# Kernel optimization log

Hardware: AMD Instinct MI355X
Metric: run time of the kernel (lower is better)

The kernel has to match this reference:

```python
import jax, jax.numpy as jnp
import numpy as np

V, T, E, H, B, S = 50000, 45, 256, 512, 32, 256


def setup_inputs() -> dict:
    key = jax.random.key(0)
    ks = jax.random.split(key, 14)
    s = 0.05
    return dict(
        x=jax.random.randint(ks[0], (B, S), 0, V),
        tags=jax.random.randint(ks[1], (B, S), 0, T),
        mask=jnp.ones((B, S), dtype=bool),
        emb=jax.random.normal(ks[2], (V, E), jnp.float32),
        Wih_f=jax.random.normal(ks[3], (4 * H, E), jnp.float32) * s,
        Whh_f=jax.random.normal(ks[4], (4 * H, H), jnp.float32) * s,
        bih_f=jnp.zeros((4 * H,), jnp.float32),
        bhh_f=jnp.zeros((4 * H,), jnp.float32),
        Wih_b=jax.random.normal(ks[5], (4 * H, E), jnp.float32) * s,
        Whh_b=jax.random.normal(ks[6], (4 * H, H), jnp.float32) * s,
        bih_b=jnp.zeros((4 * H,), jnp.float32),
        bhh_b=jnp.zeros((4 * H,), jnp.float32),
        Wout=jax.random.normal(ks[7], (T, 2 * H), jnp.float32) * s,
        bout=jnp.zeros((T,), jnp.float32),
        start=jax.random.normal(ks[8], (T,), jnp.float32) * 0.1,
        end=jax.random.normal(ks[9], (T,), jnp.float32) * 0.1,
        trans=jax.random.normal(ks[10], (T, T), jnp.float32) * 0.1,
    )


def _lstm_dir(xp, Whh, reverse):
    # xp: [S, B, 4H] precomputed input projection + biases; gate order i,f,g,o (torch)
    Bn = xp.shape[1]
    Hn = Whh.shape[1]
    def step(carry, g_in):
        h, c = carry
        g = g_in + h @ Whh.T
        i, f, gg, o = jnp.split(g, 4, axis=-1)
        c = jax.nn.sigmoid(f) * c + jax.nn.sigmoid(i) * jnp.tanh(gg)
        h = jax.nn.sigmoid(o) * jnp.tanh(c)
        return (h, c), h
    init = (jnp.zeros((Bn, Hn), xp.dtype), jnp.zeros((Bn, Hn), xp.dtype))
    _, hs = jax.lax.scan(step, init, xp, reverse=reverse)
    return hs  # [S, B, H]


def _crf_nll(emissions, tags, mask, start, end, trans):
    # emissions: [B, S, T]; neg mean log-likelihood (torchcrf, reduction='mean')
    mf = mask.astype(emissions.dtype)
    em_tag = jnp.take_along_axis(emissions, tags[:, :, None], axis=2)[:, :, 0]  # [B,S]
    num = start[tags[:, 0]] + em_tag[:, 0]
    num = num + ((trans[tags[:, :-1], tags[:, 1:]] + em_tag[:, 1:]) * mf[:, 1:]).sum(1)
    seq_ends = mf.sum(1).astype(tags.dtype) - 1
    last_tags = jnp.take_along_axis(tags, seq_ends[:, None], axis=1)[:, 0]
    num = num + end[last_tags]
    def denom_step(alpha, inp):
        em_t, m_t = inp  # [B,T], [B]
        nxt = jax.nn.logsumexp(alpha[:, :, None] + trans[None, :, :] + em_t[:, None, :], axis=1)
        return jnp.where(m_t[:, None] > 0, nxt, alpha), None
    alpha0 = start[None, :] + emissions[:, 0]
    em_rest = emissions.transpose(1, 0, 2)[1:]  # [S-1, B, T]
    alpha, _ = jax.lax.scan(denom_step, alpha0, (em_rest, mf.T[1:]))
    logZ = jax.nn.logsumexp(alpha + end[None, :], axis=1)
    return -(num - logZ).mean()


def reference(x, tags, mask, emb, Wih_f, Whh_f, bih_f, bhh_f,
              Wih_b, Whh_b, bih_b, bhh_b, Wout, bout, start, end, trans):
    embeds = emb[x]                      # [B, S, E]
    xs = embeds.transpose(1, 0, 2)       # [S, B, E]
    xp_f = jnp.einsum('sbe,ge->sbg', xs, Wih_f) + bih_f + bhh_f
    hs_f = _lstm_dir(xp_f, Whh_f, False)
    xp_b = jnp.einsum('sbe,ge->sbg', xs, Wih_b) + bih_b + bhh_b
    hs_b = _lstm_dir(xp_b, Whh_b, True)
    hcat = jnp.concatenate([hs_f, hs_b], axis=-1)          # [S, B, 2H]
    emissions = jnp.einsum('sbh,th->sbt', hcat, Wout) + bout
    emissions = emissions.transpose(1, 0, 2)                # [B, S, T]
    return _crf_nll(emissions, tags, mask, start, end, trans)
```

## Files before the change

### kernel.cpp

```cpp
#include <hip/hip_runtime.h>
#include <stdint.h>

#define S_LEN 256
#define B_N 32
#define H_N 512
#define E_N 256
#define T_N 45
#define G4H 2048

typedef unsigned short u16;
typedef unsigned int u32;
typedef u16 u16x8 __attribute__((ext_vector_type(8)));
typedef u16 u16x4 __attribute__((ext_vector_type(4)));
typedef u32 u32x4 __attribute__((ext_vector_type(4)));
typedef u32 u32x2 __attribute__((ext_vector_type(2)));
typedef __bf16 bf16x8 __attribute__((ext_vector_type(8)));
typedef float f32x4 __attribute__((ext_vector_type(4)));
typedef unsigned long long u64;

#define OFF_ATOK  256ull
#define OFF_WIHF  (OFF_ATOK + 4194304ull)
#define OFF_WIHB  (OFF_WIHF + 1048576ull)
#define OFF_WHHF  (OFF_WIHB + 1048576ull)
#define OFF_WHHB  (OFF_WHHF + 2097152ull)
#define OFF_WOUT  (OFF_WHHB + 2097152ull)
#define OFF_BSF   (OFF_WOUT + 98304ull)
#define OFF_BSB   (OFF_BSF + 8192ull)
#define OFF_XPF   (OFF_BSB + 8192ull)
#define OFF_XPB   (OFF_XPF + 33554432ull)
#define OFF_HSF   (OFF_XPB + 33554432ull)
#define OFF_HSB   (OFF_HSF + 8421376ull)
#define OFF_EM    (OFF_HSB + 8421376ull)

__device__ __forceinline__ u16 f2bf(float f) {
  union { float f; unsigned u; } v; v.f = f;
  unsigned r = v.u + 0x7FFFu + ((v.u >> 16) & 1u);
  return (u16)(r >> 16);
}
__device__ __forceinline__ float bf2f(u16 b) {
  union { unsigned u; float f; } v; v.u = ((unsigned)b) << 16;
  return v.f;
}
__device__ __forceinline__ bf16x8 ld8(const u16* p) {
  u16x8 v = *reinterpret_cast<const u16x8*>(p);
  return __builtin_bit_cast(bf16x8, v);
}
__device__ __forceinline__ void st_h8cc(u16* p, u16x4 v) {
  __hip_atomic_store(reinterpret_cast<u64*>(p), __builtin_bit_cast(u64, v),
                     __ATOMIC_RELAXED, __HIP_MEMORY_SCOPE_AGENT);
}
__device__ __forceinline__ u32x4 ld16cc(const u16* p) {
  u32x4 r;
  asm volatile("global_load_dwordx4 %0, %1, off sc1"
               : "=v"(r) : "v"(p) : "memory");
  return r;
}
__device__ __forceinline__ u32x2 ld8cc(const u16* p) {
  u32x2 r;
  asm volatile("global_load_dwordx2 %0, %1, off sc1"
               : "=v"(r) : "v"(p) : "memory");
  return r;
}
__device__ __forceinline__ u32 ld4cc(const float* p) {
  u32 r;
  asm volatile("global_load_dword %0, %1, off sc1"
               : "=v"(r) : "v"(p) : "memory");
  return r;
}
__device__ __forceinline__ void st2cc(u16* p, u32 v) {
  asm volatile("global_store_short %0, %1, off sc1"
               :: "v"(p), "v"(v) : "memory");
}
__device__ __forceinline__ void st4cc(float* p, float v) {
  asm volatile("global_store_dword %0, %1, off sc1"
               :: "v"(p), "v"(__builtin_bit_cast(u32, v)) : "memory");
}
__device__ __forceinline__ f32x4 mfma16(bf16x8 a, bf16x8 b, f32x4 c) {
  return __builtin_amdgcn_mfma_f32_16x16x32_bf16(a, b, c, 0, 0, 0);
}
__device__ __forceinline__ float sigm(float x) { return 1.f / (1.f + __expf(-x)); }
__device__ __forceinline__ float tanhf_(float x) {
  float ax = fabsf(x);
  float e = __expf(-2.f * ax);
  float t = 1.f - 2.f * e / (1.f + e);
  return (x < 0.f) ? -t : t;
}
__device__ __forceinline__ float wredmax(float v) {
  #pragma unroll
  for (int m = 1; m < 64; m <<= 1) v = fmaxf(v, __shfl_xor(v, m));
  return v;
}
__device__ __forceinline__ float wredsum(float v) {
  #pragma unroll
  for (int m = 1; m < 64; m <<= 1) v += __shfl_xor(v, m);
  return v;
}

__global__ void k_castAW(const int* __restrict__ x, const float* __restrict__ emb,
                         u16* __restrict__ atok,
                         const float* __restrict__ WihF, const float* __restrict__ WihB,
                         const float* __restrict__ WhhF, const float* __restrict__ WhhB,
                         const float* __restrict__ Wout,
                         const float* __restrict__ bihF, const float* __restrict__ bhhF,
                         const float* __restrict__ bihB, const float* __restrict__ bhhB,
                         u16* wihf, u16* wihb, u16* whhf, u16* whhb, u16* woutp,
                         float* bsf, float* bsb, u16* hsf, u16* hsb,
                         u16* hsfill, u16* xpfill, float* emfill, float* outp) {
  int bid = blockIdx.x;
  if (bid >= 34512) { if (threadIdx.x == 0) *outp = 0.f; return; }
  u32x4 sent = {0xFFFFFFFFu, 0xFFFFFFFFu, 0xFFFFFFFFu, 0xFFFFFFFFu};
  if (bid >= 34128) {
    reinterpret_cast<u32x4*>(emfill)[(size_t)(bid - 34128) * 256 + threadIdx.x] = sent;
    return;
  }
  if (bid >= 17744) {
    reinterpret_cast<u32x4*>(xpfill)[(size_t)(bid - 17744) * 256 + threadIdx.x] = sent;
    return;
  }
  if (bid >= 13648) {
    reinterpret_cast<u32x4*>(hsfill)[(size_t)(bid - 13648) * 256 + threadIdx.x] = sent;
    return;
  }
  if (bid < 1024) {
    int idx = bid * 256 + threadIdx.x;
    int t = idx >> 5;
    int e0 = (idx & 31) << 3;
    int s = t >> 5, b = t & 31;
    int xid = x[b * S_LEN + s];
    const float4* p = reinterpret_cast<const float4*>(emb + (size_t)xid * E_N + e0);
    float4 lo = p[0], hi = p[1];
    u16x8 o;
    o[0] = f2bf(lo.x); o[1] = f2bf(lo.y); o[2] = f2bf(lo.z); o[3] = f2bf(lo.w);
    o[4] = f2bf(hi.x); o[5] = f2bf(hi.y); o[6] = f2bf(hi.z); o[7] = f2bf(hi.w);
    *reinterpret_cast<u16x8*>(atok + (size_t)t * E_N + e0) = o;
    return;
  }
  int i = (bid - 1024) * 256 + threadIdx.x;
  if (i < 524288) { wihf[i] = f2bf(WihF[i]); return; }
  i -= 524288;
  if (i < 524288) { wihb[i] = f2bf(WihB[i]); return; }
  i -= 524288;
  if (i < 1048576) { whhf[i] = f2bf(WhhF[i]); return; }
  i -= 1048576;
  if (i < 1048576) { whhb[i] = f2bf(WhhB[i]); return; }
  i -= 1048576;
  if (i < 49152) {
    int n = i >> 10, k = i & 1023;
    woutp[i] = (n < T_N) ? f2bf(Wout[n * 1024 + k]) : (u16)0;
    return;
  }
  i -= 49152;
  if (i < 2048) { bsf[i] = bihF[i] + bhhF[i]; return; }
  i -= 2048;
  if (i < 2048) { bsb[i] = bihB[i] + bhhB[i]; return; }
  i -= 2048;
  if (i < 16384) { hsf[i] = 0; return; }
  i -= 16384;
  if (i < 16384) { hsb[(size_t)256 * 16384 + i] = 0; return; }
}

__global__ __launch_bounds__(128, 1) void k_fused(
    const u16* __restrict__ whhF, const u16* __restrict__ whhB,
    const u16* __restrict__ atok,
    const u16* __restrict__ wihF, const u16* __restrict__ wihB,
    const float* __restrict__ bsF, const float* __restrict__ bsB,
    u16* __restrict__ xpF, u16* __restrict__ xpB,
    u16* __restrict__ hsF, u16* __restrict__ hsB,
    const u16* __restrict__ woutp, const float* __restrict__ bout,
    float* __restrict__ em, const int* __restrict__ tags,
    const float* __restrict__ startv, const float* __restrict__ endv,
    const float* __restrict__ trans, float* __restrict__ out) {
  __shared__ float tl[T_N * T_N + 64];
  const int bid = (int)blockIdx.x;
  if (bid >= 64 && bid < 4160) {
    int j = bid - 64;
    int dir = j & 1, idx = j >> 1;
    int tIdx = idx >> 4, gIdx = idx & 15;
    if (dir) tIdx = 127 - tIdx;
    const int wave = threadIdx.x >> 6, lane = threadIdx.x & 63;
    const int lr = lane & 15, lh = lane >> 4;
    const int t0 = tIdx * 64;
    const int g0 = gIdx * 128 + wave * 64;
    const u16* wih = dir ? wihB : wihF;
    const float* bs = dir ? bsB : bsF;
    u16* xp = dir ? xpB : xpF;
    f32x4 acc[4][4] = {};
    for (int kk = 0; kk < 8; ++kk) {
      int e = kk * 32 + lh * 8;
      bf16x8 a[4], bfr[4];
      #pragma unroll
      for (int mi = 0; mi < 4; ++mi) a[mi] = ld8(atok + (size_t)(t0 + 16 * mi + lr) * E_N + e);
      #pragma unroll
      for (int ni = 0; ni < 4; ++ni) bfr[ni] = ld8(wih + (size_t)(g0 + 16 * ni + lr) * E_N + e);
      #pragma unroll
      for (int mi = 0; mi < 4; ++mi)
        #pragma unroll
        for (int ni = 0; ni < 4; ++ni) acc[mi][ni] = mfma16(a[mi], bfr[ni], acc[mi][ni]);
    }
    #pragma unroll
    for (int ni = 0; ni < 4; ++ni) {
      int g = g0 + 16 * ni + lr;
      float bsv = bs[g];
      #pragma unroll
      for (int mi = 0; mi < 4; ++mi)
        #pragma unroll
        for (int r = 0; r < 4; ++r) {
          int t = t0 + 16 * mi + 4 * lh + r;
          st2cc(xp + (size_t)t * G4H + g, (u32)f2bf(acc[mi][ni][r] + bsv));
        }
    }
    return;
  }
  if (bid >= 4160 && bid < 4416) {
    const int s = bid - 4160;
    const int wv = threadIdx.x >> 6, lane = threadIdx.x & 63;
    const int lr = lane & 15, lh = lane >> 4;
    const int b = wv * 16 + lr;
    const u16* af = hsF + ((size_t)(s + 1) * B_N + b) * H_N + lh * 8;
    const u16* ab = hsB + ((size_t)s * B_N + b) * H_N + lh * 8;
    for (;;) {
      u32x4 c0 = ld16cc(af);
      u32x4 c1 = ld16cc(ab);
      asm volatile("s_waitcnt vmcnt(0)" ::: "memory");
      __builtin_amdgcn_sched_barrier(0);
      u32 bad = (c0[0] == 0xFFFFFFFFu) | (c0[2] == 0xFFFFFFFFu) |
                (c1[0] == 0xFFFFFFFFu) | (c1[2] == 0xFFFFFFFFu);
      if (!__builtin_amdgcn_ballot_w64(bad != 0u)) break;
      __builtin_amdgcn_s_sleep(32);
    }
    u32x4 raw[32];
    #pragma unroll
    for (int kk = 0; kk < 16; ++kk) raw[kk] = ld16cc(af + kk * 32);
    #pragma unroll
    for (int kk = 0; kk < 16; ++kk) raw[16 + kk] = ld16cc(ab + kk * 32);
    asm volatile("s_waitcnt vmcnt(0)" ::: "memory");
    __builtin_amdgcn_sched_barrier(0);
    u32 pend = 0;
    #pragma unroll
    for (int kk = 0; kk < 32; ++kk)
      if (raw[kk][0] == 0xFFFFFFFFu || raw[kk][2] == 0xFFFFFFFFu) pend |= (1u << kk);
    while (__builtin_amdgcn_ballot_w64(pend != 0u)) {
      __builtin_amdgcn_s_sleep(1);
      #pragma unroll
      for (int kk = 0; kk < 16; ++kk)
        if (pend & (1u << kk)) raw[kk] = ld16cc(af + kk * 32);
      #pragma unroll
      for (int kk = 0; kk < 16; ++kk)
        if (pend & (1u << (16 + kk))) raw[16 + kk] = ld16cc(ab + kk * 32);
      asm volatile("s_waitcnt vmcnt(0)" ::: "memory");
      __builtin_amdgcn_sched_barrier(0);
      u32 np = 0;
      #pragma unroll
      for (int kk = 0; kk < 32; ++kk)
        if ((pend & (1u << kk)) &&
            (raw[kk][0] == 0xFFFFFFFFu || raw[kk][2] == 0xFFFFFFFFu)) np |= (1u << kk);
      pend = np;
    }
    f32x4 acc[3] = {};
    #pragma unroll
    for (int kk = 0; kk < 32; ++kk) {
      int k = kk * 32 + lh * 8;
      bf16x8 a = __builtin_bit_cast(bf16x8, raw[kk]);
      #pragma unroll
      for (int ni = 0; ni < 3; ++ni) {
        bf16x8 bb = ld8(woutp + (size_t)(16 * ni + lr) * 1024 + k);
        acc[ni] = mfma16(a, bb, acc[ni]);
      }
    }
    #pragma unroll
    for (int ni = 0; ni < 3; ++ni) {
      int tag = 16 * ni + lr;
      float bo = (tag < T_N) ? bout[tag] : 0.f;
      #pragma unroll
      for (int r = 0; r < 4; ++r) {
        int t = s * 32 + wv * 16 + 4 * lh + r;
        st4cc(em + (size_t)t * 48 + tag, acc[ni][r] + bo);
      }
    }
    return;
  }
  if (bid >= 4416) {
    const int cb = bid - 4416;
    const int wv = threadIdx.x >> 6, lane = threadIdx.x & 63;
    const int b = cb * 2 + wv;
    for (int i = threadIdx.x; i < T_N * T_N + 64; i += 128)
      tl[i] = (i < T_N * T_N) ? trans[i] : 0.f;
    __syncthreads();
    u32 ev = 0u;
    {
      const float* row = em + (size_t)b * 48;
      for (;;) {
        if (lane < 48) ev = ld4cc(row + lane);
        asm volatile("s_waitcnt vmcnt(0)" ::: "memory");
        __builtin_amdgcn_sched_barrier(0);
        if (!__builtin_amdgcn_ballot_w64(lane < 48 && ev == 0xFFFFFFFFu)) break;
        __builtin_amdgcn_s_sleep(32);
      }
    }
    float acur = (lane < T_N) ? (startv[lane] + __builtin_bit_cast(float, ev)) : -1e30f;
    u32 evn = 0u;
    if (lane < 48) evn = ld4cc(em + (size_t)(32 + b) * 48 + lane);
    for (int s = 1; s < S_LEN; ++s) {
      asm volatile("s_waitcnt vmcnt(0)" ::: "memory");
      __builtin_amdgcn_sched_barrier(0);
      while (__builtin_amdgcn_ballot_w64(lane < 48 && evn == 0xFFFFFFFFu)) {
        __builtin_amdgcn_s_sleep(32);
        if (lane < 48) evn = ld4cc(em + ((size_t)s * 32 + b) * 48 + lane);
        asm volatile("s_waitcnt vmcnt(0)" ::: "memory");
        __builtin_amdgcn_sched_barrier(0);
      }
      float emv = __builtin_bit_cast(float, evn);
      if (s < S_LEN - 1 && lane < 48)
        evn = ld4cc(em + ((size_t)(s + 1) * 32 + b) * 48 + lane);
      float shift = wredmax(acur);
      float s0 = 0.f, s1 = 0.f, s2 = 0.f;
      #pragma unroll
      for (int t = 0; t < T_N; t += 3) {
        s0 += __expf(__shfl(acur, t)     + tl[t * T_N + lane]       - shift);
        s1 += __expf(__shfl(acur, t + 1) + tl[(t + 1) * T_N + lane] - shift);
        s2 += __expf(__shfl(acur, t + 2) + tl[(t + 2) * T_N + lane] - shift);
      }
      acur = (lane < T_N) ? (shift + __logf(s0 + s1 + s2) + emv) : -1e30f;
    }
    float z = (lane < T_N) ? (acur + endv[lane]) : -1e30f;
    float m = wredmax(z);
    float sum = wredsum((lane < T_N) ? __expf(z - m) : 0.f);
    float logZ = m + __logf(sum);
    u32 g[4]; float tlv[4];
    #pragma unroll
    for (int q = 0; q < 4; ++q) {
      int s = 1 + lane * 4 + q;
      g[q] = 0u; tlv[q] = 0.f;
      if (s < S_LEN) {
        int tp = tags[b * S_LEN + s - 1], tc = tags[b * S_LEN + s];
        tlv[q] = tl[tp * T_N + tc];
        g[q] = ld4cc(em + ((size_t)s * 32 + b) * 48 + tc);
      }
    }
    asm volatile("s_waitcnt vmcnt(0)" ::: "memory");
    __builtin_amdgcn_sched_barrier(0);
    float np = 0.f;
    #pragma unroll
    for (int q = 0; q < 4; ++q) {
      int s = 1 + lane * 4 + q;
      if (s < S_LEN) np += tlv[q] + __builtin_bit_cast(float, g[q]);
    }
    np = wredsum(np);
    if (lane == 0) {
      int tg0 = tags[b * S_LEN], tgL = tags[b * S_LEN + S_LEN - 1];
      u32 e0 = ld4cc(em + (size_t)b * 48 + tg0);
      asm volatile("s_waitcnt vmcnt(0)" ::: "memory");
      __builtin_amdgcn_sched_barrier(0);
      float num = startv[tg0] + __builtin_bit_cast(float, e0) + np + endv[tgL];
      atomicAdd(out, -(num - logZ) / (float)B_N);
    }
    return;
  }
  const int dir = bid >> 5;
  const int w = bid & 31;
  const int nt = threadIdx.x >> 6;
  const int lane = threadIdx.x & 63;
  const int lr = lane & 15, lh = lane >> 4;
  const u16* whh = dir ? whhB : whhF;
  const u16* xp = dir ? xpB : xpF;
  u16* hs = dir ? hsB : hsF;

  bf16x8 A[4][16];
  #pragma unroll
  for (int mt = 0; mt < 4; ++mt) {
    const u16* base = whh + (size_t)(mt * 512 + 16 * w + lr) * H_N + lh * 8;
    #pragma unroll
    for (int kk = 0; kk < 16; ++kk) A[mt][kk] = ld8(base + kk * 32);
  }
  const int b = nt * 16 + lr;
  const int j0 = 16 * w + 4 * lh;
  float cst[4] = {0.f, 0.f, 0.f, 0.f};

  for (int t = 0; t < S_LEN; ++t) {
    const int s = dir ? (S_LEN - 1 - t) : t;
    const int slot_r = dir ? (s + 1) : s;
    const int slot_w = dir ? s : (s + 1);

    u32x2 xqr[4];
    const u16* xpt = xp + ((size_t)(s * B_N + b)) * G4H + j0;
    #pragma unroll
    for (int mt = 0; mt < 4; ++mt) xqr[mt] = ld8cc(xpt + mt * 512);

    const u16* hp = hs + ((size_t)slot_r * B_N + b) * H_N + lh * 8;
    u32x4 raw[16];
    #pragma unroll
    for (int kk = 0; kk < 16; ++kk) raw[kk] = ld16cc(hp + kk * 32);
    asm volatile("s_waitcnt vmcnt(0)" ::: "memory");
    __builtin_amdgcn_sched_barrier(0);
    u32 pend = 0;
    #pragma unroll
    for (int kk = 0; kk < 16; ++kk)
      if (raw[kk][0] == 0xFFFFFFFFu || raw[kk][2] == 0xFFFFFFFFu) pend |= (1u << kk);
    while (__builtin_amdgcn_ballot_w64(pend != 0u)) {
      __builtin_amdgcn_s_sleep(1);
      #pragma unroll
      for (int kk = 0; kk < 16; ++kk)
        if (pend & (1u << kk)) raw[kk] = ld16cc(hp + kk * 32);
      asm volatile("s_waitcnt vmcnt(0)" ::: "memory");
      __builtin_amdgcn_sched_barrier(0);
      u32 np = 0;
      #pragma unroll
      for (int kk = 0; kk < 16; ++kk)
        if ((pend & (1u << kk)) &&
            (raw[kk][0] == 0xFFFFFFFFu || raw[kk][2] == 0xFFFFFFFFu)) np |= (1u << kk);
      pend = np;
    }

    f32x4 acc[4] = {};
    #pragma unroll
    for (int kk = 0; kk < 16; ++kk) {
      bf16x8 Bf = __builtin_bit_cast(bf16x8, raw[kk]);
      #pragma unroll
      for (int mt = 0; mt < 4; ++mt) acc[mt] = mfma16(A[mt][kk], Bf, acc[mt]);
    }

    for (;;) {
      u32 xbad = 0;
      #pragma unroll
      for (int mt = 0; mt < 4; ++mt) {
        #pragma unroll
        for (int d = 0; d < 2; ++d) {
          u32 wv = xqr[mt][d];
          xbad |= ((wv & 0xFFFFu) == 0xFFFFu) | ((wv >> 16) == 0xFFFFu);
        }
      }
      if (!__builtin_amdgcn_ballot_w64(xbad != 0u)) break;
      __builtin_amdgcn_s_sleep(1);
      #pragma unroll
      for (int mt = 0; mt < 4; ++mt) xqr[mt] = ld8cc(xpt + mt * 512);
      asm volatile("s_waitcnt vmcnt(0)" ::: "memory");
      __builtin_amdgcn_sched_barrier(0);
    }

    u16x4 hv;
    #pragma unroll
    for (int r = 0; r < 4; ++r) {
      u32 w0 = xqr[0][r >> 1], w1 = xqr[1][r >> 1], w2 = xqr[2][r >> 1], w3 = xqr[3][r >> 1];
      u16 x0 = (r & 1) ? (u16)(w0 >> 16) : (u16)(w0 & 0xFFFFu);
      u16 x1 = (r & 1) ? (u16)(w1 >> 16) : (u16)(w1 & 0xFFFFu);
      u16 x2 = (r & 1) ? (u16)(w2 >> 16) : (u16)(w2 & 0xFFFFu);
      u16 x3 = (r & 1) ? (u16)(w3 >> 16) : (u16)(w3 & 0xFFFFu);
      float gi = acc[0][r] + bf2f(x0);
      float gf = acc[1][r] + bf2f(x1);
      float gg = acc[2][r] + bf2f(x2);
      float go = acc[3][r] + bf2f(x3);
      float c = sigm(gf) * cst[r] + sigm(gi) * tanhf_(gg);
      cst[r] = c;
      hv[r] = f2bf(sigm(go) * tanhf_(c));
    }
    st_h8cc(hs + ((size_t)slot_w * B_N + b) * H_N + j0, hv);
  }
}

extern "C" void kernel_launch(void* const* d_in, const int* in_sizes, int n_in,
                              void* d_out, int out_size, void* d_ws, size_t ws_size,
                              hipStream_t stream) {
  const int* x = (const int*)d_in[0];
  const int* tags = (const int*)d_in[1];
  const float* emb = (const float*)d_in[3];
  const float* WihF = (const float*)d_in[4];
  const float* WhhF = (const float*)d_in[5];
  const float* bihF = (const float*)d_in[6];
  const float* bhhF = (const float*)d_in[7];
  const float* WihB = (const float*)d_in[8];
  const float* WhhB = (const float*)d_in[9];
  const float* bihB = (const float*)d_in[10];
  const float* bhhB = (const float*)d_in[11];
  const float* Wout = (const float*)d_in[12];
  const float* bout = (const float*)d_in[13];
  const float* startv = (const float*)d_in[14];
  const float* endv = (const float*)d_in[15];
  const float* trans = (const float*)d_in[16];
  float* out = (float*)d_out;
  char* ws = (char*)d_ws;

  u16* atok = (u16*)(ws + OFF_ATOK);
  u16* wihf = (u16*)(ws + OFF_WIHF);
  u16* wihb = (u16*)(ws + OFF_WIHB);
  u16* whhf = (u16*)(ws + OFF_WHHF);
  u16* whhb = (u16*)(ws + OFF_WHHB);
  u16* woutp = (u16*)(ws + OFF_WOUT);
  float* bsf = (float*)(ws + OFF_BSF);
  float* bsb = (float*)(ws + OFF_BSB);
  u16* xpf = (u16*)(ws + OFF_XPF);
  u16* xpb = (u16*)(ws + OFF_XPB);
  u16* hsf = (u16*)(ws + OFF_HSF);
  u16* hsb = (u16*)(ws + OFF_HSB);
  float* emis = (float*)(ws + OFF_EM);
  u16* hsfill = (u16*)(ws + OFF_HSF + 32768ull);

  k_castAW<<<34513, 256, 0, stream>>>(x, emb, atok, WihF, WihB, WhhF, WhhB, Wout,
                                      bihF, bhhF, bihB, bhhB,
                                      wihf, wihb, whhf, whhb, woutp, bsf, bsb, hsf, hsb,
                                      hsfill, xpf, emis, out);
  k_fused<<<4432, 128, 0, stream>>>(whhf, whhb, atok, wihf, wihb, bsf, bsb,
                                    xpf, xpb, hsf, hsb,
                                    woutp, bout, emis, tags, startv, endv, trans, out);
}
```

Before: 1.548 ms.

## Split emission and CRF stages out of persistent fused kernel into separate launch

Moves the emission projection and CRF forward blocks out of the fused LSTM kernel into a new second kernel launched after the recurrence completes. The emission blocks no longer spin-wait on hidden-state sentinels, since the hidden states are complete at launch. The CRF blocks still poll emission rows, now with a shorter sleep. This removes spinning blocks that competed with the recurrent LSTM blocks for CUs during the recurrence. The cost is that emission/CRF work no longer overlaps with the LSTM, and an extra launch is added.

New measurement: 1.547 ms. Within noise of the previous version (-0.1%).

```diff
diff --git a/kernel.cpp b/kernel.cpp
--- a/kernel.cpp
+++ b/kernel.cpp
@@ -165,15 +165,9 @@
     const u16* __restrict__ wihF, const u16* __restrict__ wihB,
     const float* __restrict__ bsF, const float* __restrict__ bsB,
     u16* __restrict__ xpF, u16* __restrict__ xpB,
-    u16* __restrict__ hsF, u16* __restrict__ hsB,
-    const u16* __restrict__ woutp, const float* __restrict__ bout,
-    float* __restrict__ em, const int* __restrict__ tags,
-    const float* __restrict__ startv, const float* __restrict__ endv,
-    const float* __restrict__ trans, float* __restrict__ out) {
-  __shared__ float tl[T_N * T_N + 64];
-  const int bid = (int)blockIdx.x;
-  if (bid >= 64 && bid < 4160) {
-    int j = bid - 64;
+    u16* __restrict__ hsF, u16* __restrict__ hsB) {
+  if (blockIdx.x >= 64) {
+    int j = (int)blockIdx.x - 64;
     int dir = j & 1, idx = j >> 1;
     int tIdx = idx >> 4, gIdx = idx & 15;
     if (dir) tIdx = 127 - tIdx;
@@ -211,153 +205,8 @@
     }
     return;
   }
-  if (bid >= 4160 && bid < 4416) {
-    const int s = bid - 4160;
-    const int wv = threadIdx.x >> 6, lane = threadIdx.x & 63;
-    const int lr = lane & 15, lh = lane >> 4;
-    const int b = wv * 16 + lr;
-    const u16* af = hsF + ((size_t)(s + 1) * B_N + b) * H_N + lh * 8;
-    const u16* ab = hsB + ((size_t)s * B_N + b) * H_N + lh * 8;
-    for (;;) {
-      u32x4 c0 = ld16cc(af);
-      u32x4 c1 = ld16cc(ab);
-      asm volatile("s_waitcnt vmcnt(0)" ::: "memory");
-      __builtin_amdgcn_sched_barrier(0);
-      u32 bad = (c0[0] == 0xFFFFFFFFu) | (c0[2] == 0xFFFFFFFFu) |
-                (c1[0] == 0xFFFFFFFFu) | (c1[2] == 0xFFFFFFFFu);
-      if (!__builtin_amdgcn_ballot_w64(bad != 0u)) break;
-      __builtin_amdgcn_s_sleep(32);
-    }
-    u32x4 raw[32];
-    #pragma unroll
-    for (int kk = 0; kk < 16; ++kk) raw[kk] = ld16cc(af + kk * 32);
-    #pragma unroll
-    for (int kk = 0; kk < 16; ++kk) raw[16 + kk] = ld16cc(ab + kk * 32);
-    asm volatile("s_waitcnt vmcnt(0)" ::: "memory");
-    __builtin_amdgcn_sched_barrier(0);
-    u32 pend = 0;
-    #pragma unroll
-    for (int kk = 0; kk < 32; ++kk)
-      if (raw[kk][0] == 0xFFFFFFFFu || raw[kk][2] == 0xFFFFFFFFu) pend |= (1u << kk);
-    while (__builtin_amdgcn_ballot_w64(pend != 0u)) {
-      __builtin_amdgcn_s_sleep(1);
-      #pragma unroll
-      for (int kk = 0; kk < 16; ++kk)
-        if (pend & (1u << kk)) raw[kk] = ld16cc(af + kk * 32);
-      #pragma unroll
-      for (int kk = 0; kk < 16; ++kk)
-        if (pend & (1u << (16 + kk))) raw[16 + kk] = ld16cc(ab + kk * 32);
-      asm volatile("s_waitcnt vmcnt(0)" ::: "memory");
-      __builtin_amdgcn_sched_barrier(0);
-      u32 np = 0;
-      #pragma unroll
-      for (int kk = 0; kk < 32; ++kk)
-        if ((pend & (1u << kk)) &&
-            (raw[kk][0] == 0xFFFFFFFFu || raw[kk][2] == 0xFFFFFFFFu)) np |= (1u << kk);
-      pend = np;
-    }
-    f32x4 acc[3] = {};
-    #pragma unroll
-    for (int kk = 0; kk < 32; ++kk) {
-      int k = kk * 32 + lh * 8;
-      bf16x8 a = __builtin_bit_cast(bf16x8, raw[kk]);
-      #pragma unroll
-      for (int ni = 0; ni < 3; ++ni) {
-        bf16x8 bb = ld8(woutp + (size_t)(16 * ni + lr) * 1024 + k);
-        acc[ni] = mfma16(a, bb, acc[ni]);
-      }
-    }
-    #pragma unroll
-    for (int ni = 0; ni < 3; ++ni) {
-      int tag = 16 * ni + lr;
-      float bo = (tag < T_N) ? bout[tag] : 0.f;
-      #pragma unroll
-      for (int r = 0; r < 4; ++r) {
-        int t = s * 32 + wv * 16 + 4 * lh + r;
-        st4cc(em + (size_t)t * 48 + tag, acc[ni][r] + bo);
-      }
-    }
-    return;
-  }
-  if (bid >= 4416) {
-    const int cb = bid - 4416;
-    const int wv = threadIdx.x >> 6, lane = threadIdx.x & 63;
-    const int b = cb * 2 + wv;
-    for (int i = threadIdx.x; i < T_N * T_N + 64; i += 128)
-      tl[i] = (i < T_N * T_N) ? trans[i] : 0.f;
-    __syncthreads();
-    u32 ev = 0u;
-    {
-      const float* row = em + (size_t)b * 48;
-      for (;;) {
-        if (lane < 48) ev = ld4cc(row + lane);
-        asm volatile("s_waitcnt vmcnt(0)" ::: "memory");
-        __builtin_amdgcn_sched_barrier(0);
-        if (!__builtin_amdgcn_ballot_w64(lane < 48 && ev == 0xFFFFFFFFu)) break;
-        __builtin_amdgcn_s_sleep(32);
-      }
-    }
-    float acur = (lane < T_N) ? (startv[lane] + __builtin_bit_cast(float, ev)) : -1e30f;
-    u32 evn = 0u;
-    if (lane < 48) evn = ld4cc(em + (size_t)(32 + b) * 48 + lane);
-    for (int s = 1; s < S_LEN; ++s) {
-      asm volatile("s_waitcnt vmcnt(0)" ::: "memory");
-      __builtin_amdgcn_sched_barrier(0);
-      while (__builtin_amdgcn_ballot_w64(lane < 48 && evn == 0xFFFFFFFFu)) {
-        __builtin_amdgcn_s_sleep(32);
-        if (lane < 48) evn = ld4cc(em + ((size_t)s * 32 + b) * 48 + lane);
-        asm volatile("s_waitcnt vmcnt(0)" ::: "memory");
-        __builtin_amdgcn_sched_barrier(0);
-      }
-      float emv = __builtin_bit_cast(float, evn);
-      if (s < S_LEN - 1 && lane < 48)
-        evn = ld4cc(em + ((size_t)(s + 1) * 32 + b) * 48 + lane);
-      float shift = wredmax(acur);
-      float s0 = 0.f, s1 = 0.f, s2 = 0.f;
-      #pragma unroll
-      for (int t = 0; t < T_N; t += 3) {
-        s0 += __expf(__shfl(acur, t)     + tl[t * T_N + lane]       - shift);
-        s1 += __expf(__shfl(acur, t + 1) + tl[(t + 1) * T_N + lane] - shift);
-        s2 += __expf(__shfl(acur, t + 2) + tl[(t + 2) * T_N + lane] - shift);
-      }
-      acur = (lane < T_N) ? (shift + __logf(s0 + s1 + s2) + emv) : -1e30f;
-    }
-    float z = (lane < T_N) ? (acur + endv[lane]) : -1e30f;
-    float m = wredmax(z);
-    float sum = wredsum((lane < T_N) ? __expf(z - m) : 0.f);
-    float logZ = m + __logf(sum);
-    u32 g[4]; float tlv[4];
-    #pragma unroll
-    for (int q = 0; q < 4; ++q) {
-      int s = 1 + lane * 4 + q;
-      g[q] = 0u; tlv[q] = 0.f;
-      if (s < S_LEN) {
-        int tp = tags[b * S_LEN + s - 1], tc = tags[b * S_LEN + s];
-        tlv[q] = tl[tp * T_N + tc];
-        g[q] = ld4cc(em + ((size_t)s * 32 + b) * 48 + tc);
-      }
-    }
-    asm volatile("s_waitcnt vmcnt(0)" ::: "memory");
-    __builtin_amdgcn_sched_barrier(0);
-    float np = 0.f;
-    #pragma unroll
-    for (int q = 0; q < 4; ++q) {
-      int s = 1 + lane * 4 + q;
-      if (s < S_LEN) np += tlv[q] + __builtin_bit_cast(float, g[q]);
-    }
-    np = wredsum(np);
-    if (lane == 0) {
-      int tg0 = tags[b * S_LEN], tgL = tags[b * S_LEN + S_LEN - 1];
-      u32 e0 = ld4cc(em + (size_t)b * 48 + tg0);
-      asm volatile("s_waitcnt vmcnt(0)" ::: "memory");
-      __builtin_amdgcn_sched_barrier(0);
-      float num = startv[tg0] + __builtin_bit_cast(float, e0) + np + endv[tgL];
-      atomicAdd(out, -(num - logZ) / (float)B_N);
-    }
-    return;
-  }
-  const int dir = bid >> 5;
-  const int w = bid & 31;
+  const int dir = blockIdx.x >> 5;
+  const int w = blockIdx.x & 31;
   const int nt = threadIdx.x >> 6;
   const int lane = threadIdx.x & 63;
   const int lr = lane & 15, lh = lane >> 4;
@@ -454,6 +303,120 @@
       hv[r] = f2bf(sigm(go) * tanhf_(c));
     }
     st_h8cc(hs + ((size_t)slot_w * B_N + b) * H_N + j0, hv);
+  }
+}
+
+__global__ __launch_bounds__(128) void k_emcrf(
+    const u16* __restrict__ hsF, const u16* __restrict__ hsB,
+    const u16* __restrict__ woutp, const float* __restrict__ bout,
+    float* __restrict__ em, const int* __restrict__ tags,
+    const float* __restrict__ startv, const float* __restrict__ endv,
+    const float* __restrict__ trans, float* __restrict__ out) {
+  __shared__ float tl[T_N * T_N + 64];
+  const int bid = (int)blockIdx.x;
+  if (bid < 256) {
+    const int s = bid;
+    const int wv = threadIdx.x >> 6, lane = threadIdx.x & 63;
+    const int lr = lane & 15, lh = lane >> 4;
+    const int b = wv * 16 + lr;
+    const u16* af = hsF + ((size_t)(s + 1) * B_N + b) * H_N + lh * 8;
+    const u16* ab = hsB + ((size_t)s * B_N + b) * H_N + lh * 8;
+    f32x4 acc[3] = {};
+    #pragma unroll
+    for (int kk = 0; kk < 32; ++kk) {
+      int k = kk * 32 + lh * 8;
+      bf16x8 a = (kk < 16) ? ld8(af + kk * 32) : ld8(ab + (kk - 16) * 32);
+      #pragma unroll
+      for (int ni = 0; ni < 3; ++ni) {
+        bf16x8 bb = ld8(woutp + (size_t)(16 * ni + lr) * 1024 + k);
+        acc[ni] = mfma16(a, bb, acc[ni]);
+      }
+    }
+    #pragma unroll
+    for (int ni = 0; ni < 3; ++ni) {
+      int tag = 16 * ni + lr;
+      float bo = (tag < T_N) ? bout[tag] : 0.f;
+      #pragma unroll
+      for (int r = 0; r < 4; ++r) {
+        int t = s * 32 + wv * 16 + 4 * lh + r;
+        st4cc(em + (size_t)t * 48 + tag, acc[ni][r] + bo);
+      }
+    }
+    return;
+  }
+  const int cb = bid - 256;
+  const int wv = threadIdx.x >> 6, lane = threadIdx.x & 63;
+  const int b = cb * 2 + wv;
+  for (int i = threadIdx.x; i < T_N * T_N + 64; i += 128)
+    tl[i] = (i < T_N * T_N) ? trans[i] : 0.f;
+  __syncthreads();
+  u32 ev = 0u;
+  {
+    const float* row = em + (size_t)b * 48;
+    for (;;) {
+      if (lane < 48) ev = ld4cc(row + lane);
+      asm volatile("s_waitcnt vmcnt(0)" ::: "memory");
+      __builtin_amdgcn_sched_barrier(0);
+      if (!__builtin_amdgcn_ballot_w64(lane < 48 && ev == 0xFFFFFFFFu)) break;
+      __builtin_amdgcn_s_sleep(16);
+    }
+  }
+  float acur = (lane < T_N) ? (startv[lane] + __builtin_bit_cast(float, ev)) : -1e30f;
+  u32 evn = 0u;
+  if (lane < 48) evn = ld4cc(em + (size_t)(32 + b) * 48 + lane);
+  for (int s = 1; s < S_LEN; ++s) {
+    asm volatile("s_waitcnt vmcnt(0)" ::: "memory");
+    __builtin_amdgcn_sched_barrier(0);
+    while (__builtin_amdgcn_ballot_w64(lane < 48 && evn == 0xFFFFFFFFu)) {
+      __builtin_amdgcn_s_sleep(16);
+      if (lane < 48) evn = ld4cc(em + ((size_t)s * 32 + b) * 48 + lane);
+      asm volatile("s_waitcnt vmcnt(0)" ::: "memory");
+      __builtin_amdgcn_sched_barrier(0);
+    }
+    float emv = __builtin_bit_cast(float, evn);
+    if (s < S_LEN - 1 && lane < 48)
+      evn = ld4cc(em + ((size_t)(s + 1) * 32 + b) * 48 + lane);
+    float shift = wredmax(acur);
+    float s0 = 0.f, s1 = 0.f, s2 = 0.f;
+    #pragma unroll
+    for (int t = 0; t < T_N; t += 3) {
+      s0 += __expf(__shfl(acur, t)     + tl[t * T_N + lane]       - shift);
+      s1 += __expf(__shfl(acur, t + 1) + tl[(t + 1) * T_N + lane] - shift);
+      s2 += __expf(__shfl(acur, t + 2) + tl[(t + 2) * T_N + lane] - shift);
+    }
+    acur = (lane < T_N) ? (shift + __logf(s0 + s1 + s2) + emv) : -1e30f;
+  }
+  float z = (lane < T_N) ? (acur + endv[lane]) : -1e30f;
+  float m = wredmax(z);
+  float sum = wredsum((lane < T_N) ? __expf(z - m) : 0.f);
+  float logZ = m + __logf(sum);
+  u32 g[4]; float tlv[4];
+  #pragma unroll
+  for (int q = 0; q < 4; ++q) {
+    int s = 1 + lane * 4 + q;
+    g[q] = 0u; tlv[q] = 0.f;
+    if (s < S_LEN) {
+      int tp = tags[b * S_LEN + s - 1], tc = tags[b * S_LEN + s];
+      tlv[q] = tl[tp * T_N + tc];
+      g[q] = ld4cc(em + ((size_t)s * 32 + b) * 48 + tc);
+    }
+  }
+  asm volatile("s_waitcnt vmcnt(0)" ::: "memory");
+  __builtin_amdgcn_sched_barrier(0);
+  float np = 0.f;
+  #pragma unroll
+  for (int q = 0; q < 4; ++q) {
+    int s = 1 + lane * 4 + q;
+    if (s < S_LEN) np += tlv[q] + __builtin_bit_cast(float, g[q]);
+  }
+  np = wredsum(np);
+  if (lane == 0) {
+    int tg0 = tags[b * S_LEN], tgL = tags[b * S_LEN + S_LEN - 1];
+    u32 e0 = ld4cc(em + (size_t)b * 48 + tg0);
+    asm volatile("s_waitcnt vmcnt(0)" ::: "memory");
+    __builtin_amdgcn_sched_barrier(0);
+    float num = startv[tg0] + __builtin_bit_cast(float, e0) + np + endv[tgL];
+    atomicAdd(out, -(num - logZ) / (float)B_N);
   }
 }
 
@@ -498,7 +461,8 @@
                                       bihF, bhhF, bihB, bhhB,
                                       wihf, wihb, whhf, whhb, woutp, bsf, bsb, hsf, hsb,
                                       hsfill, xpf, emis, out);
-  k_fused<<<4432, 128, 0, stream>>>(whhf, whhb, atok, wihf, wihb, bsf, bsb,
-                                    xpf, xpb, hsf, hsb,
-                                    woutp, bout, emis, tags, startv, endv, trans, out);
-}
+  k_fused<<<4160, 128, 0, stream>>>(whhf, whhb, atok, wihf, wihb, bsf, bsb,
+                                    xpf, xpb, hsf, hsb);
+  k_emcrf<<<272, 128, 0, stream>>>(hsf, hsb, woutp, bout, emis, tags,
+                                   startv, endv, trans, out);
+}
```
